# Optimization experiments

Hardware: AMD Instinct MI355X
Metric: run time of the kernel (lower is better)

Reference implementation:

```python
import jax, jax.numpy as jnp
import numpy as np

HEADS = 8
DIM_HEAD = 64
DIM = 128
TOPK = (8, 8, 8)  # depth, height, width


def chan_ln(x, g, b):
    # channel layernorm over axis=1 (biased variance), eps added to std
    mean = jnp.mean(x, axis=1, keepdims=True)
    var = jnp.var(x, axis=1, keepdims=True)
    return g * (x - mean) / (jnp.sqrt(var) + 1e-6) + b


def l2norm(x):
    # F.normalize(dim=1): divide by max(||x||_2, eps)
    n = jnp.sqrt(jnp.sum(x * x, axis=1, keepdims=True))
    return x / jnp.maximum(n, 1e-12)


def _forward(query_source, context, w_q, w_kv, w_out,
             ctx_gamma, ctx_beta, qs_gamma, qs_beta, out_gamma, out_beta, gamma):
    b, c, Dq, Hq, Wq = query_source.shape
    Dc, Hc, Wc = context.shape[2:]
    kd, kh, kw = TOPK

    ctx = chan_ln(context, ctx_gamma, ctx_beta)
    qs = chan_ln(query_source, qs_gamma, qs_beta)

    # 1x1x1 convs == channel matmuls
    kv = jnp.einsum('bcdhw,oc->bodhw', ctx, w_kv)   # (b, 2*inner, D, H, W)
    k, v = jnp.split(kv, 2, axis=1)
    q = jnp.einsum('bcdhw,oc->bodhw', qs, w_q)      # (b, inner, D, H, W)

    def fold(t):  # (b, h*c, D,H,W) -> (b*h, c, D,H,W)
        return t.reshape(b * HEADS, DIM_HEAD, *t.shape[2:])

    q, k, v = fold(q), fold(k), fold(v)
    q, k = l2norm(q), l2norm(k)

    q_probe = jnp.sum(q, axis=(2, 3, 4))            # (bh, c)
    k_abs = jnp.abs(k)

    if kd < Dc:
        score = jnp.einsum('bc,bcd->bd', q_probe, jnp.sum(k_abs, axis=(3, 4)))
        idx = jax.lax.top_k(score, kd)[1][:, None, :, None, None]
        k = jnp.take_along_axis(k, idx, axis=2)
        v = jnp.take_along_axis(v, idx, axis=2)
    if kh < Hc:
        score = jnp.einsum('bc,bch->bh', q_probe, jnp.sum(k_abs, axis=(2, 4)))
        idx = jax.lax.top_k(score, kh)[1][:, None, None, :, None]
        k = jnp.take_along_axis(k, idx, axis=3)
        v = jnp.take_along_axis(v, idx, axis=3)
    if kw < Wc:
        score = jnp.einsum('bc,bcw->bw', q_probe, jnp.sum(k_abs, axis=(2, 3)))
        idx = jax.lax.top_k(score, kw)[1][:, None, None, None, :]
        k = jnp.take_along_axis(k, idx, axis=4)
        v = jnp.take_along_axis(v, idx, axis=4)

    def flat(t):  # (bh, c, d, h, w) -> (bh, d*h*w, c)
        return t.reshape(t.shape[0], t.shape[1], -1).transpose(0, 2, 1)

    qf, kf, vf = flat(q), flat(k), flat(v)
    sim = jnp.einsum('bic,bjc->bij', qf, kf)        # (bh, Nq, Nkv)
    attn = jax.nn.softmax(sim, axis=-1)
    out = jnp.einsum('bij,bjc->bic', attn, vf)      # (bh, Nq, c)

    out = out.reshape(b, HEADS, Dq, Hq, Wq, DIM_HEAD)
    out = out.transpose(0, 1, 5, 2, 3, 4).reshape(b, HEADS * DIM_HEAD, Dq, Hq, Wq)
    out = jnp.einsum('bcdhw,oc->bodhw', out, w_out)
    out = chan_ln(out, out_gamma, out_beta)
    return gamma * out + query_source


def setup_inputs() -> dict:
    key = jax.random.key(0)
    ks = jax.random.split(key, 6)
    b, c, D, H, W = 2, DIM, 16, 32, 32
    inner = HEADS * DIM_HEAD
    ones = jnp.ones((1, c, 1, 1, 1), jnp.float32)
    zeros = jnp.zeros((1, c, 1, 1, 1), jnp.float32)
    return {
        'query_source': jax.random.normal(ks[0], (b, c, D, H, W), jnp.float32),
        'context': jax.random.normal(ks[1], (b, c, D, H, W), jnp.float32),
        'w_q': jax.random.normal(ks[2], (inner, c), jnp.float32) / np.sqrt(c).astype(np.float32),
        'w_kv': jax.random.normal(ks[3], (2 * inner, c), jnp.float32) / np.sqrt(c).astype(np.float32),
        'w_out': jax.random.normal(ks[4], (c, inner), jnp.float32) / np.sqrt(inner).astype(np.float32),
        'ctx_gamma': ones, 'ctx_beta': zeros,
        'qs_gamma': ones, 'qs_beta': zeros,
        'out_gamma': ones, 'out_beta': zeros,
        'gamma': jnp.full((1,), 0.5, jnp.float32),
    }


def reference(query_source, context, w_q, w_kv, w_out,
              ctx_gamma, ctx_beta, qs_gamma, qs_beta, out_gamma, out_beta, gamma):
    return _forward(query_source, context, w_q, w_kv, w_out,
                    ctx_gamma, ctx_beta, qs_gamma, qs_beta, out_gamma, out_beta, gamma)
```

## Files before the change

### kernel.cpp

```cpp
#include <hip/hip_runtime.h>
#include <hip/hip_bf16.h>

#define S_SP 16384
#define NKV 512

typedef short short8 __attribute__((ext_vector_type(8)));
typedef float v4f   __attribute__((ext_vector_type(4)));

__device__ __forceinline__ unsigned short f2bf(float x){
  union { float f; unsigned u; } v; v.f = x;
  unsigned r = v.u + 0x7FFFu + ((v.u >> 16) & 1u);
  return (unsigned short)(r >> 16);
}
__device__ __forceinline__ float bf2f(unsigned short h){
  union { unsigned u; float f; } v; v.u = ((unsigned)h) << 16; return v.f;
}

#if defined(__has_builtin)
#if __has_builtin(__builtin_amdgcn_cvt_pk_bf16_f32)
#define HAVE_PKBF 1
#endif
#endif

__device__ __forceinline__ unsigned pk2(float a, float b){
#ifdef HAVE_PKBF
  typedef __bf16 bf16x2 __attribute__((ext_vector_type(2)));
  union { bf16x2 v; unsigned u; } r;
  r.v = __builtin_amdgcn_cvt_pk_bf16_f32(a, b);
  return r.u;
#else
  return (unsigned)f2bf(a) | ((unsigned)f2bf(b) << 16);
#endif
}

__device__ __forceinline__ short8 u2s8(uint4 u){
  union { uint4 u; short8 s; } x; x.u = u; return x.s;
}

__global__ __launch_bounds__(256) void k_stats(const float* __restrict__ ctx,
                                               const float* __restrict__ qs,
                                               const float* __restrict__ ctx_g,
                                               const float* __restrict__ ctx_b,
                                               const float* __restrict__ qs_g,
                                               const float* __restrict__ qs_b,
                                               const float* __restrict__ wq,
                                               const float* __restrict__ wkv,
                                               float* __restrict__ MEAN,
                                               float* __restrict__ INV,
                                               unsigned short* __restrict__ XTC_hi,
                                               unsigned short* __restrict__ XTC_lo,
                                               unsigned short* __restrict__ XTQ_hi,
                                               unsigned short* __restrict__ XTQ_lo,
                                               unsigned short* __restrict__ WQh,
                                               unsigned short* __restrict__ WQl,
                                               unsigned short* __restrict__ WKh,
                                               unsigned short* __restrict__ WKl){
  __shared__ float r1[4][64];
  __shared__ float r2[4][64];
  __shared__ float mb[64], ib[64];
  __shared__ __align__(16) unsigned short TH[64*136];
  __shared__ __align__(16) unsigned short TL[64*136];
  int bx = blockIdx.x;
  int t = threadIdx.x;
  if (bx >= 1024){
    int wb = bx - 1024;
    int isK = wb >> 5;
    size_t i8 = ((size_t)(wb & 31)*256 + t)*8;
    const float* srcw = isK ? wkv : wq;
    unsigned short* dh = isK ? WKh : WQh;
    unsigned short* dl = isK ? WKl : WQl;
    v4f a  = *(const v4f*)(srcw + i8);
    v4f b2 = *(const v4f*)(srcw + i8 + 4);
    unsigned short h[8], l[8];
    #pragma unroll
    for (int i=0;i<4;i++){
      h[i]   = f2bf(a[i]);  l[i]   = f2bf(a[i]  - bf2f(h[i]));
      h[i+4] = f2bf(b2[i]); l[i+4] = f2bf(b2[i] - bf2f(h[i+4]));
    }
    uint4 uh, ul;
    uh.x = (unsigned)h[0] | ((unsigned)h[1]<<16);
    uh.y = (unsigned)h[2] | ((unsigned)h[3]<<16);
    uh.z = (unsigned)h[4] | ((unsigned)h[5]<<16);
    uh.w = (unsigned)h[6] | ((unsigned)h[7]<<16);
    ul.x = (unsigned)l[0] | ((unsigned)l[1]<<16);
    ul.y = (unsigned)l[2] | ((unsigned)l[3]<<16);
    ul.z = (unsigned)l[4] | ((unsigned)l[5]<<16);
    ul.w = (unsigned)l[6] | ((unsigned)l[7]<<16);
    *(uint4*)(dh + i8) = uh;
    *(uint4*)(dl + i8) = ul;
    return;
  }
  int tt = bx >> 9; int b = (bx >> 8) & 1; int sc = bx & 255;
  int sv = t & 63, cg = t >> 6;
  int s = sc*64 + sv;
  const float* src = (tt ? qs : ctx) + ((size_t)b*128 + cg*32)*S_SP + s;
  const float* G  = tt ? qs_g : ctx_g;
  const float* Bv = tt ? qs_b : ctx_b;
  float xv[32];
  float sum = 0.f, ss = 0.f;
  #pragma unroll
  for (int c = 0; c < 32; c++){
    float v = src[(size_t)c*S_SP];
    xv[c] = v;
    sum += v; ss += v*v;
  }
  r1[cg][sv] = sum; r2[cg][sv] = ss;
  __syncthreads();
  if (t < 64){
    float sm = r1[0][t]+r1[1][t]+r1[2][t]+r1[3][t];
    float sq = r2[0][t]+r2[1][t]+r2[2][t]+r2[3][t];
    float mean = sm * 0.0078125f;
    float var  = fmaxf(sq * 0.0078125f - mean*mean, 0.f);
    float inv  = 1.f/(sqrtf(var) + 1e-6f);
    int o = tt*2*S_SP + b*S_SP + sc*64 + t;
    MEAN[o] = mean; INV[o] = inv;
    mb[t] = mean; ib[t] = inv;
  }
  __syncthreads();
  float m = mb[sv], iv = ib[sv];
  #pragma unroll
  for (int i = 0; i < 32; i += 2){
    int c = cg*32 + i;
    float y0 = G[c]  *(xv[i]  -m)*iv + Bv[c];
    float y1 = G[c+1]*(xv[i+1]-m)*iv + Bv[c+1];
    unsigned short h0 = f2bf(y0), h1 = f2bf(y1);
    unsigned short l0 = f2bf(y0 - bf2f(h0)), l1 = f2bf(y1 - bf2f(h1));
    *(unsigned*)&TH[sv*136 + c] = (unsigned)h0 | ((unsigned)h1 << 16);
    *(unsigned*)&TL[sv*136 + c] = (unsigned)l0 | ((unsigned)l1 << 16);
  }
  __syncthreads();
  int row = t >> 2, seg = (t & 3) * 32;
  unsigned short* XH = tt ? XTQ_hi : XTC_hi;
  unsigned short* XL = tt ? XTQ_lo : XTC_lo;
  size_t go = ((size_t)b*S_SP + sc*64 + row)*128 + seg;
  #pragma unroll
  for (int k2 = 0; k2 < 4; k2++){
    *(uint4*)(XH + go + k2*8) = *(const uint4*)&TH[row*136 + seg + k2*8];
    *(uint4*)(XL + go + k2*8) = *(const uint4*)&TL[row*136 + seg + k2*8];
  }
}

template<int ISK>
__global__ __launch_bounds__(256, 2) void k_proj(
    const unsigned short* __restrict__ XH, const unsigned short* __restrict__ XL,
    const unsigned short* __restrict__ WH, const unsigned short* __restrict__ WL,
    unsigned short* __restrict__ QBF, float* __restrict__ QP,
    float* __restrict__ SCORE){
  __shared__ float qpl[128];
  __shared__ float qacc[128];
  __shared__ float wacc[64];
  int bx = blockIdx.x;
  int og = bx >> 7, b = (bx >> 6) & 1, stile = bx & 63;
  int t = threadIdx.x, wvi = t >> 6, lane = t & 63;
  int quad = lane >> 4, l15 = lane & 15;
  int sw0 = stile*256 + wvi*64;
  int bh0 = b*8 + og*2;
  if (ISK){
    if (t < 128) qpl[t] = QP[bh0*64 + t];
    if (t < 64) wacc[t] = 0.f;
    __syncthreads();
  } else {
    if (t < 128) qacc[t] = 0.f;
  }
  v4f acc[8][4];
  #pragma unroll
  for (int i=0;i<8;i++)
    #pragma unroll
    for (int j=0;j<4;j++) acc[i][j] = (v4f){0.f,0.f,0.f,0.f};
  size_t wrow = ((size_t)(og*128 + l15))*128 + quad*8;
  size_t xrow = ((size_t)b*S_SP + sw0 + l15)*128 + quad*8;
  #pragma unroll 1
  for (int ks=0; ks<4; ks++){
    int ko = ks*32;
    uint4 bhv[4], blv[4], av[8];
    #pragma unroll
    for (int nt=0;nt<4;nt++){
      bhv[nt] = *(const uint4*)(XH + xrow + nt*2048 + ko);
      blv[nt] = *(const uint4*)(XL + xrow + nt*2048 + ko);
    }
    #pragma unroll
    for (int mt=0;mt<8;mt++) av[mt] = *(const uint4*)(WH + wrow + mt*2048 + ko);
    #pragma unroll
    for (int mt=0;mt<8;mt++){
      short8 am = u2s8(av[mt]);
      #pragma unroll
      for (int nt=0;nt<4;nt++)
        acc[mt][nt] = __builtin_amdgcn_mfma_f32_16x16x32_bf16(am, u2s8(bhv[nt]), acc[mt][nt], 0, 0, 0);
      #pragma unroll
      for (int nt=0;nt<4;nt++)
        acc[mt][nt] = __builtin_amdgcn_mfma_f32_16x16x32_bf16(am, u2s8(blv[nt]), acc[mt][nt], 0, 0, 0);
    }
    #pragma unroll
    for (int mt=0;mt<8;mt++){
      short8 am = u2s8(*(const uint4*)(WL + wrow + mt*2048 + ko));
      #pragma unroll
      for (int nt=0;nt<4;nt++)
        acc[mt][nt] = __builtin_amdgcn_mfma_f32_16x16x32_bf16(am, u2s8(bhv[nt]), acc[mt][nt], 0, 0, 0);
    }
  }
  float inv0[4], inv1[4];
  #pragma unroll
  for (int nt=0;nt<4;nt++){
    float p0 = 0.f, p1 = 0.f;
    #pragma unroll
    for (int mt=0;mt<4;mt++)
      #pragma unroll
      for (int r=0;r<4;r++){
        p0 += acc[mt][nt][r]*acc[mt][nt][r];
        p1 += acc[mt+4][nt][r]*acc[mt+4][nt][r];
      }
    p0 += __shfl_xor(p0,16,64); p0 += __shfl_xor(p0,32,64);
    p1 += __shfl_xor(p1,16,64); p1 += __shfl_xor(p1,32,64);
    inv0[nt] = 1.f/fmaxf(sqrtf(p0),1e-12f);
    inv1[nt] = 1.f/fmaxf(sqrtf(p1),1e-12f);
  }
  if (!ISK){
    #pragma unroll
    for (int mt=0;mt<8;mt++)
      #pragma unroll
      for (int nt=0;nt<4;nt++){
        float iv = (mt<4) ? inv0[nt] : inv1[nt];
        #pragma unroll
        for (int r=0;r<4;r++) acc[mt][nt][r] *= iv;
      }
    #pragma unroll
    for (int mt=0;mt<8;mt++){
      int bh = bh0 + (mt>>2);
      #pragma unroll
      for (int nt=0;nt<4;nt++){
        int s = sw0 + nt*16 + l15;
        uint2 wv;
        wv.x = pk2(acc[mt][nt][0], acc[mt][nt][1]);
        wv.y = pk2(acc[mt][nt][2], acc[mt][nt][3]);
        *(uint2*)(QBF + ((size_t)bh*S_SP + s)*64 + (mt&3)*16 + quad*4) = wv;
      }
    }
    __syncthreads();
    #pragma unroll
    for (int mt=0;mt<8;mt++){
      #pragma unroll
      for (int r=0;r<4;r++){
        float v = acc[mt][0][r]+acc[mt][1][r]+acc[mt][2][r]+acc[mt][3][r];
        v += __shfl_xor(v,1,64); v += __shfl_xor(v,2,64);
        v += __shfl_xor(v,4,64); v += __shfl_xor(v,8,64);
        if (l15 == 0)
          atomicAdd(&qacc[(mt>>2)*64 + (mt&3)*16 + quad*4 + r], v);
      }
    }
    __syncthreads();
    if (t < 128) atomicAdd(QP + bh0*64 + t, qacc[t]);
  } else {
    float v0[4] = {0,0,0,0}, v1[4] = {0,0,0,0};
    #pragma unroll
    for (int mt=0;mt<8;mt++){
      #pragma unroll
      for (int r=0;r<4;r++){
        float w = qpl[mt*16 + quad*4 + r];
        #pragma unroll
        for (int nt=0;nt<4;nt++){
          float av = fabsf(acc[mt][nt][r]) * w;
          if (mt < 4) v0[nt] += av; else v1[nt] += av;
        }
      }
    }
    #pragma unroll
    for (int nt=0;nt<4;nt++){
      v0[nt] += __shfl_xor(v0[nt],16,64); v0[nt] += __shfl_xor(v0[nt],32,64);
      v1[nt] += __shfl_xor(v1[nt],16,64); v1[nt] += __shfl_xor(v1[nt],32,64);
      v0[nt] *= inv0[nt]; v1[nt] *= inv1[nt];
    }
    float w00 = v0[0]+v0[2], w10 = v0[1]+v0[3];
    float w01 = v1[0]+v1[2], w11 = v1[1]+v1[3];
    float h00 = v0[0]+v0[1], h01 = v0[2]+v0[3];
    float h10 = v1[0]+v1[1], h11 = v1[2]+v1[3];
    #pragma unroll
    for (int mm=1; mm<16; mm<<=1){
      h00 += __shfl_xor(h00,mm,64); h01 += __shfl_xor(h01,mm,64);
      h10 += __shfl_xor(h10,mm,64); h11 += __shfl_xor(h11,mm,64);
    }
    if (lane < 16){
      atomicAdd(&wacc[l15],      w00);
      atomicAdd(&wacc[16+l15],   w10);
      atomicAdd(&wacc[32+l15],   w01);
      atomicAdd(&wacc[48+l15],   w11);
    }
    if (lane == 0){
      int hb = 16 + (stile&3)*8 + wvi*2;
      atomicAdd(SCORE + bh0*80 + hb,     h00);
      atomicAdd(SCORE + bh0*80 + hb + 1, h01);
      atomicAdd(SCORE + (bh0+1)*80 + hb,     h10);
      atomicAdd(SCORE + (bh0+1)*80 + hb + 1, h11);
      atomicAdd(SCORE + bh0*80 + (stile>>2), h00+h01);
      atomicAdd(SCORE + (bh0+1)*80 + (stile>>2), h10+h11);
    }
    __syncthreads();
    if (t < 64) atomicAdd(SCORE + (bh0 + (t>>5))*80 + 48 + (t&31), wacc[t]);
  }
}

__global__ __launch_bounds__(64) void k_topk(const float* __restrict__ SCORE,
                                             int* __restrict__ IDX){
  int bh = blockIdx.x;
  if (threadIdx.x != 0) return;
  float sc[80];
  for (int i=0;i<80;i++) sc[i] = SCORE[bh*80+i];
  for (int a=0;a<3;a++){
    int n = a ? 32 : 16;
    int off = (a==0) ? 0 : (a==1 ? 16 : 48);
    for (int it=0; it<8; it++){
      int bi = 0; float bv = -3.4e38f;
      for (int i=0;i<n;i++){ float v = sc[off+i]; if (v > bv){ bv=v; bi=i; } }
      IDX[bh*24 + a*8 + it] = bi;
      sc[off+bi] = -3.4e38f;
    }
  }
}

__global__ __launch_bounds__(256) void k_gather(const float* __restrict__ ctx,
    const float* __restrict__ wkv, const float* __restrict__ ctx_g,
    const float* __restrict__ ctx_b, const float* __restrict__ MEAN,
    const float* __restrict__ INV, const int* __restrict__ IDX,
    unsigned short* __restrict__ KG, unsigned short* __restrict__ VGT){
  __shared__ float wlds[64*129];
  __shared__ float xln[32*128];
  __shared__ int sidx[24];
  int bx = blockIdx.x;
  int bh = bx >> 5, jc = (bx >> 1) & 15, type = bx & 1;
  int head = bh & 7, b = bh >> 3;
  int t = threadIdx.x;
  if (t < 24) sidx[t] = IDX[bh*24 + t];
  {
    int oc = t>>2, ks = (t&3)*32;
    const float* wr = wkv + ((size_t)(type*512 + head*64 + oc))*128 + ks;
    #pragma unroll 8
    for (int i=0;i<32;i++) wlds[oc*129 + ks + i] = wr[i];
  }
  __syncthreads();
  {
    int jl = t>>3, seg = (t&7)*16;
    int jj = jc*32 + jl;
    int dsel = sidx[jj>>6], hsel = sidx[8 + ((jj>>3)&7)], wsel = sidx[16 + (jj&7)];
    int sj = dsel*1024 + hsel*32 + wsel;
    float mn = MEAN[b*S_SP + sj];
    float iv = INV[b*S_SP + sj];
    #pragma unroll
    for (int i=0;i<16;i++){
      int cc = seg + i;
      float raw = ctx[((size_t)(b*128 + cc))*S_SP + sj];
      xln[jl*128 + cc] = ctx_g[cc]*(raw - mn)*iv + ctx_b[cc];
    }
  }
  __syncthreads();
  int c = t & 63, jg = t >> 6;
  float accv[8] = {};
  #pragma unroll 4
  for (int k=0;k<128;k++){
    float wv = wlds[c*129 + k];
    #pragma unroll
    for (int m=0;m<8;m++) accv[m] += wv * xln[(jg + 4*m)*128 + k];
  }
  #pragma unroll
  for (int m=0;m<8;m++){
    int jj = jc*32 + jg + 4*m;
    float a = accv[m];
    if (type == 0){
      float sq = a*a;
      #pragma unroll
      for (int mm=32; mm; mm>>=1) sq += __shfl_xor(sq, mm, 64);
      float rn = 1.f/fmaxf(sqrtf(sq), 1e-12f);
      KG[((size_t)bh*NKV + jj)*64 + c] = f2bf(a*rn);
    } else {
      VGT[((size_t)bh*64 + c)*NKV + jj] = f2bf(a);
    }
  }
}

__global__ __launch_bounds__(256) void k_attn(const unsigned short* __restrict__ QBF,
    const unsigned short* __restrict__ KG, const unsigned short* __restrict__ VGT,
    unsigned short* __restrict__ AOUT){
  __shared__ __align__(16) unsigned short kst[128*72];
  __shared__ __align__(16) unsigned short vst[64*136];
  __shared__ __align__(16) unsigned short pst[4][64*40];
  int bx = blockIdx.x;
  int bh = bx >> 6, qb = bx & 63;
  int t = threadIdx.x;
  int wvi = t >> 6, lane = t & 63;
  int quad = lane >> 4, l15 = lane & 15;
  int q0 = qb*256 + wvi*64;
  const unsigned short* kgb = KG + (size_t)bh*NKV*64;
  const unsigned short* vgb = VGT + (size_t)bh*64*NKV;
  short8 bq[4][2];
  #pragma unroll
  for (int qt=0; qt<4; qt++){
    const unsigned short* qp_ = QBF + ((size_t)bh*S_SP + q0 + qt*16 + l15)*64 + quad*8;
    union { uint4 u; short8 s; } u0, u1;
    u0.u = *(const uint4*)(qp_);
    u1.u = *(const uint4*)(qp_ + 32);
    bq[qt][0] = u0.s; bq[qt][1] = u1.s;
  }
  v4f oacc[4][4];
  #pragma unroll
  for (int i=0;i<4;i++)
    #pragma unroll
    for (int j=0;j<4;j++) oacc[i][j] = (v4f){0.f,0.f,0.f,0.f};
  float lsum[4] = {0.f,0.f,0.f,0.f};
  unsigned short* pw = pst[wvi];
  for (int ch=0; ch<4; ch++){
    __syncthreads();
    {
      int jl = t>>1, hf = (t&1)*32;
      const unsigned short* sp = kgb + (size_t)(ch*128 + jl)*64 + hf;
      unsigned short* dp = kst + jl*72 + hf;
      #pragma unroll
      for (int i=0;i<4;i++) *(uint4*)(dp + i*8) = *(const uint4*)(sp + i*8);
    }
    {
      int cc = t>>2, js = (t&3)*32;
      const unsigned short* sp = vgb + (size_t)cc*NKV + ch*128 + js;
      unsigned short* dp = vst + cc*136 + js;
      #pragma unroll
      for (int i=0;i<4;i++) *(uint4*)(dp + i*8) = *(const uint4*)(sp + i*8);
    }
    __syncthreads();
    #pragma unroll
    for (int sub=0; sub<4; sub++){
      v4f s[2][4];
      #pragma unroll
      for (int j2=0; j2<2; j2++){
        int jt = sub*2 + j2;
        const unsigned short* kr = kst + (jt*16 + l15)*72 + quad*8;
        union { uint4 u; short8 s; } a0, a1;
        a0.u = *(const uint4*)(kr);
        a1.u = *(const uint4*)(kr + 32);
        #pragma unroll
        for (int qt=0; qt<4; qt++){
          v4f z = {0.f,0.f,0.f,0.f};
          z = __builtin_amdgcn_mfma_f32_16x16x32_bf16(a0.s, bq[qt][0], z, 0, 0, 0);
          z = __builtin_amdgcn_mfma_f32_16x16x32_bf16(a1.s, bq[qt][1], z, 0, 0, 0);
          s[j2][qt] = z;
        }
      }
      #pragma unroll
      for (int j2=0; j2<2; j2++){
        #pragma unroll
        for (int qt=0; qt<4; qt++){
          v4f p;
          #pragma unroll
          for (int r=0;r<4;r++) p[r] = __expf(s[j2][qt][r] - 1.0f);
          lsum[qt] += p[0]+p[1]+p[2]+p[3];
          uint2 wv;
          wv.x = pk2(p[0], p[1]);
          wv.y = pk2(p[2], p[3]);
          *(uint2*)&pw[(qt*16 + l15)*40 + j2*16 + quad*4] = wv;
        }
      }
      short8 bp[4];
      #pragma unroll
      for (int qt=0; qt<4; qt++){
        union { uint4 u; short8 s; } ub;
        ub.u = *(const uint4*)&pw[(qt*16 + l15)*40 + quad*8];
        bp[qt] = ub.s;
      }
      #pragma unroll
      for (int ct=0; ct<4; ct++){
        union { uint4 u; short8 s; } av;
        av.u = *(const uint4*)&vst[(ct*16 + l15)*136 + sub*32 + quad*8];
        #pragma unroll
        for (int qt=0; qt<4; qt++)
          oacc[ct][qt] = __builtin_amdgcn_mfma_f32_16x16x32_bf16(av.s, bp[qt], oacc[ct][qt], 0, 0, 0);
      }
    }
  }
  float rl[4];
  #pragma unroll
  for (int qt=0; qt<4; qt++){
    float l = lsum[qt];
    l += __shfl_xor(l, 16, 64);
    l += __shfl_xor(l, 32, 64);
    rl[qt] = 1.f/l;
  }
  #pragma unroll
  for (int qt=0; qt<4; qt++){
    #pragma unroll
    for (int ct=0; ct<4; ct++){
      v4f o = oacc[ct][qt];
      uint2 wv;
      wv.x = pk2(o[0]*rl[qt], o[1]*rl[qt]);
      wv.y = pk2(o[2]*rl[qt], o[3]*rl[qt]);
      *(uint2*)(AOUT + ((size_t)bh*S_SP + q0 + qt*16 + l15)*64 + ct*16 + quad*4) = wv;
    }
  }
}

__global__ __launch_bounds__(256) void k_out(const unsigned short* __restrict__ AOUT,
    const float* __restrict__ wout, const float* __restrict__ out_g,
    const float* __restrict__ out_b, const float* __restrict__ gamma,
    const float* __restrict__ qsrc, float* __restrict__ OUT){
  __shared__ __align__(16) unsigned short wl[128*40];
  __shared__ float lnp[4][2][64];
  __shared__ float mbuf[64], sbuf[64], ogl[128], obl[128];
  int bx = blockIdx.x; int b = bx>>8; int stile = bx&255; int s0 = stile*64;
  int t = threadIdx.x; int w = t>>6; int lane = t&63;
  int q = lane>>4; int l15 = lane&15;
  if (t < 128){ ogl[t] = out_g[t]; obl[t] = out_b[t]; }
  v4f acc[2][4];
  #pragma unroll
  for (int i=0;i<2;i++)
    #pragma unroll
    for (int j=0;j<4;j++) acc[i][j] = (v4f){0.f,0.f,0.f,0.f};
  for (int kt=0; kt<16; kt++){
    __syncthreads();
    {
      int c = t>>1, kb = (t&1)*16;
      const float* wr = wout + (size_t)c*512 + kt*32 + kb;
      v4f a0 = *(const v4f*)wr, a1 = *(const v4f*)(wr+4);
      v4f a2 = *(const v4f*)(wr+8), a3 = *(const v4f*)(wr+12);
      uint4 u0, u1;
      u0.x = pk2(a0[0], a0[1]); u0.y = pk2(a0[2], a0[3]);
      u0.z = pk2(a1[0], a1[1]); u0.w = pk2(a1[2], a1[3]);
      u1.x = pk2(a2[0], a2[1]); u1.y = pk2(a2[2], a2[3]);
      u1.z = pk2(a3[0], a3[1]); u1.w = pk2(a3[2], a3[3]);
      *(uint4*)&wl[c*40+kb]   = u0;
      *(uint4*)&wl[c*40+kb+8] = u1;
    }
    __syncthreads();
    short8 af[2];
    #pragma unroll
    for (int mt=0;mt<2;mt++){
      union { uint4 u; short8 s; } ua;
      ua.u = *(const uint4*)&wl[(w*32+mt*16+l15)*40 + q*8];
      af[mt] = ua.s;
    }
    int head = kt>>1; int cc0 = (kt&1)*32 + q*8;
    const unsigned short* bp = AOUT + ((size_t)((b*8+head)*S_SP + s0 + l15))*64 + cc0;
    #pragma unroll
    for (int nt=0;nt<4;nt++){
      union { uint4 u; short8 s; } ub;
      ub.u = *(const uint4*)(bp + (size_t)nt*16*64);
      #pragma unroll
      for (int mt=0;mt<2;mt++)
        acc[mt][nt] = __builtin_amdgcn_mfma_f32_16x16x32_bf16(af[mt], ub.s, acc[mt][nt], 0, 0, 0);
    }
  }
  #pragma unroll
  for (int nt=0;nt<4;nt++){
    float p1 = 0.f, p2 = 0.f;
    #pragma unroll
    for (int mt=0;mt<2;mt++)
      #pragma unroll
      for (int r=0;r<4;r++){ float v = acc[mt][nt][r]; p1 += v; p2 += v*v; }
    p1 += __shfl_xor(p1,16,64); p1 += __shfl_xor(p1,32,64);
    p2 += __shfl_xor(p2,16,64); p2 += __shfl_xor(p2,32,64);
    if (q == 0){ lnp[w][0][nt*16+l15] = p1; lnp[w][1][nt*16+l15] = p2; }
  }
  __syncthreads();
  if (t < 64){
    float m = (lnp[0][0][t]+lnp[1][0][t]+lnp[2][0][t]+lnp[3][0][t]) * 0.0078125f;
    float qq = (lnp[0][1][t]+lnp[1][1][t]+lnp[2][1][t]+lnp[3][1][t]) * 0.0078125f;
    float var = fmaxf(qq - m*m, 0.f);
    mbuf[t] = m;
    sbuf[t] = 1.f/(sqrtf(var) + 1e-6f);
  }
  __syncthreads();
  float gs = gamma[0];
  #pragma unroll
  for (int nt=0;nt<4;nt++){
    int sl = nt*16 + l15;
    float mm = mbuf[sl], ssc = sbuf[sl];
    #pragma unroll
    for (int mt=0;mt<2;mt++){
      #pragma unroll
      for (int r=0;r<4;r++){
        int c = w*32 + mt*16 + q*4 + r;
        size_t adr = ((size_t)(b*128+c))*S_SP + s0 + sl;
        float yn = (acc[mt][nt][r]-mm)*ssc;
        OUT[adr] = gs*(ogl[c]*yn + obl[c]) + qsrc[adr];
      }
    }
  }
}

extern "C" void kernel_launch(void* const* d_in, const int* in_sizes, int n_in,
                              void* d_out, int out_size, void* d_ws, size_t ws_size,
                              hipStream_t stream){
  const float* qsrc  = (const float*)d_in[0];
  const float* ctx   = (const float*)d_in[1];
  const float* wq    = (const float*)d_in[2];
  const float* wkv   = (const float*)d_in[3];
  const float* wout  = (const float*)d_in[4];
  const float* ctx_g = (const float*)d_in[5];
  const float* ctx_b = (const float*)d_in[6];
  const float* qs_g  = (const float*)d_in[7];
  const float* qs_b  = (const float*)d_in[8];
  const float* out_g = (const float*)d_in[9];
  const float* out_b = (const float*)d_in[10];
  const float* gamma = (const float*)d_in[11];
  float* OUT = (float*)d_out;
  char* ws = (char*)d_ws;
  float* QP    = (float*)(ws);
  float* SCORE = (float*)(ws + 4096);
  float* MEAN  = (float*)(ws + 16384);
  float* INV   = (float*)(ws + 278528);
  int*   IDX   = (int*)(ws + 540672);
  unsigned short* QBF  = (unsigned short*)(ws + 544768);
  unsigned short* KG   = (unsigned short*)(ws + 34099200);
  unsigned short* VGT  = (unsigned short*)(ws + 35147776);
  unsigned short* AOUT = (unsigned short*)(ws + 36196352);
  unsigned short* WQh = (unsigned short*)(ws + 34099200);
  unsigned short* WQl = (unsigned short*)(ws + 34230272);
  unsigned short* WKh = (unsigned short*)(ws + 34361344);
  unsigned short* WKl = (unsigned short*)(ws + 34492416);
  unsigned short* XTQh = (unsigned short*)(ws + 36196352);
  unsigned short* XTQl = (unsigned short*)(ws + 44584960);
  unsigned short* XTCh = (unsigned short*)(ws + 52973568);
  unsigned short* XTCl = (unsigned short*)(ws + 61362176);

  hipMemsetAsync(ws, 0, 9216, stream);
  k_stats<<<1088, 256, 0, stream>>>(ctx, qsrc, ctx_g, ctx_b, qs_g, qs_b, wq, wkv,
                                    MEAN, INV, XTCh, XTCl, XTQh, XTQl,
                                    WQh, WQl, WKh, WKl);
  k_proj<0><<<512, 256, 0, stream>>>(XTQh, XTQl, WQh, WQl, QBF, QP, SCORE);
  k_proj<1><<<512, 256, 0, stream>>>(XTCh, XTCl, WKh, WKl, QBF, QP, SCORE);
  k_topk<<<16, 64, 0, stream>>>(SCORE, IDX);
  k_gather<<<512, 256, 0, stream>>>(ctx, wkv, ctx_g, ctx_b, MEAN, INV, IDX, KG, VGT);
  k_attn<<<1024, 256, 0, stream>>>(QBF, KG, VGT, AOUT);
  k_out<<<512, 256, 0, stream>>>(AOUT, wout, out_g, out_b, gamma, qsrc, OUT);
}
```

Baseline: 304.5 us.

## Fuse top-k into gather kernel, swizzle attention LDS, raise MFMA priority

The separate single-thread top-k kernel is removed. Each gather block now recomputes the top-k indices with a wave-level shuffle argmax, which saves a launch and a serial loop at the cost of redundant work in every block. The attention kernel drops its padded LDS layouts for XOR-swizzled unpadded layouts for K, V and P, aiming to avoid bank conflicts with less shared memory. It also wraps MFMA sequences in s_setprio to favour the matrix work.

```diff
diff --git a/kernel.cpp b/kernel.cpp
--- a/kernel.cpp
+++ b/kernel.cpp
@@ -298,42 +298,46 @@
   }
 }
 
-__global__ __launch_bounds__(64) void k_topk(const float* __restrict__ SCORE,
-                                             int* __restrict__ IDX){
-  int bh = blockIdx.x;
-  if (threadIdx.x != 0) return;
-  float sc[80];
-  for (int i=0;i<80;i++) sc[i] = SCORE[bh*80+i];
-  for (int a=0;a<3;a++){
-    int n = a ? 32 : 16;
-    int off = (a==0) ? 0 : (a==1 ? 16 : 48);
-    for (int it=0; it<8; it++){
-      int bi = 0; float bv = -3.4e38f;
-      for (int i=0;i<n;i++){ float v = sc[off+i]; if (v > bv){ bv=v; bi=i; } }
-      IDX[bh*24 + a*8 + it] = bi;
-      sc[off+bi] = -3.4e38f;
-    }
-  }
-}
-
 __global__ __launch_bounds__(256) void k_gather(const float* __restrict__ ctx,
     const float* __restrict__ wkv, const float* __restrict__ ctx_g,
     const float* __restrict__ ctx_b, const float* __restrict__ MEAN,
-    const float* __restrict__ INV, const int* __restrict__ IDX,
+    const float* __restrict__ INV, const float* __restrict__ SCORE,
     unsigned short* __restrict__ KG, unsigned short* __restrict__ VGT){
   __shared__ float wlds[64*129];
   __shared__ float xln[32*128];
+  __shared__ float scb[80];
   __shared__ int sidx[24];
   int bx = blockIdx.x;
   int bh = bx >> 5, jc = (bx >> 1) & 15, type = bx & 1;
   int head = bh & 7, b = bh >> 3;
   int t = threadIdx.x;
-  if (t < 24) sidx[t] = IDX[bh*24 + t];
+  if (t < 80) scb[t] = SCORE[bh*80 + t];
   {
     int oc = t>>2, ks = (t&3)*32;
     const float* wr = wkv + ((size_t)(type*512 + head*64 + oc))*128 + ks;
     #pragma unroll 8
     for (int i=0;i<32;i++) wlds[oc*129 + ks + i] = wr[i];
+  }
+  __syncthreads();
+  if (t < 64){
+    #pragma unroll 1
+    for (int a=0;a<3;a++){
+      int n = a ? 32 : 16;
+      int off = (a==0) ? 0 : (a==1 ? 16 : 48);
+      float v = (t < n) ? scb[off+t] : -3.4e38f;
+      #pragma unroll 1
+      for (int it=0; it<8; it++){
+        float bv = v; int bi = t;
+        #pragma unroll
+        for (int mm=1; mm<32; mm<<=1){
+          float ov = __shfl_xor(bv, mm, 64);
+          int oi = __shfl_xor(bi, mm, 64);
+          if (ov > bv || (ov == bv && oi < bi)){ bv = ov; bi = oi; }
+        }
+        if (t == bi) v = -3.4e38f;
+        if (t == 0) sidx[a*8+it] = bi;
+      }
+    }
   }
   __syncthreads();
   {
@@ -378,9 +382,9 @@
 __global__ __launch_bounds__(256) void k_attn(const unsigned short* __restrict__ QBF,
     const unsigned short* __restrict__ KG, const unsigned short* __restrict__ VGT,
     unsigned short* __restrict__ AOUT){
-  __shared__ __align__(16) unsigned short kst[128*72];
-  __shared__ __align__(16) unsigned short vst[64*136];
-  __shared__ __align__(16) unsigned short pst[4][64*40];
+  __shared__ __align__(16) unsigned short kst[128*64];
+  __shared__ __align__(16) unsigned short vst[64*128];
+  __shared__ __align__(16) unsigned short pst[4][64*32];
   int bx = blockIdx.x;
   int bh = bx >> 6, qb = bx & 63;
   int t = threadIdx.x;
@@ -408,18 +412,20 @@
   for (int ch=0; ch<4; ch++){
     __syncthreads();
     {
-      int jl = t>>1, hf = (t&1)*32;
-      const unsigned short* sp = kgb + (size_t)(ch*128 + jl)*64 + hf;
-      unsigned short* dp = kst + jl*72 + hf;
-      #pragma unroll
-      for (int i=0;i<4;i++) *(uint4*)(dp + i*8) = *(const uint4*)(sp + i*8);
+      int jl = t>>1, bb = (t&1)*4;
+      const unsigned short* sp = kgb + (size_t)(ch*128 + jl)*64 + (t&1)*32;
+      unsigned short* dp = kst + jl*64;
+      int sw = jl & 7;
+      #pragma unroll
+      for (int i=0;i<4;i++) *(uint4*)(dp + (((bb+i)^sw)*8)) = *(const uint4*)(sp + i*8);
     }
     {
-      int cc = t>>2, js = (t&3)*32;
-      const unsigned short* sp = vgb + (size_t)cc*NKV + ch*128 + js;
-      unsigned short* dp = vst + cc*136 + js;
-      #pragma unroll
-      for (int i=0;i<4;i++) *(uint4*)(dp + i*8) = *(const uint4*)(sp + i*8);
+      int cc = t>>2, bb = (t&3)*4;
+      const unsigned short* sp = vgb + (size_t)cc*NKV + ch*128 + (t&3)*32;
+      unsigned short* dp = vst + cc*128;
+      int sw = cc & 7;
+      #pragma unroll
+      for (int i=0;i<4;i++) *(uint4*)(dp + (((bb+i)^sw)*8)) = *(const uint4*)(sp + i*8);
     }
     __syncthreads();
     #pragma unroll
@@ -427,11 +433,13 @@
       v4f s[2][4];
       #pragma unroll
       for (int j2=0; j2<2; j2++){
-        int jt = sub*2 + j2;
-        const unsigned short* kr = kst + (jt*16 + l15)*72 + quad*8;
+        int jr = (sub*2 + j2)*16 + l15;
+        const unsigned short* kr = kst + jr*64;
+        int sk = jr & 7;
         union { uint4 u; short8 s; } a0, a1;
-        a0.u = *(const uint4*)(kr);
-        a1.u = *(const uint4*)(kr + 32);
+        a0.u = *(const uint4*)(kr + ((quad^sk)*8));
+        a1.u = *(const uint4*)(kr + (((quad+4)^sk)*8));
+        __builtin_amdgcn_s_setprio(1);
         #pragma unroll
         for (int qt=0; qt<4; qt++){
           v4f z = {0.f,0.f,0.f,0.f};
@@ -439,6 +447,7 @@
           z = __builtin_amdgcn_mfma_f32_16x16x32_bf16(a1.s, bq[qt][1], z, 0, 0, 0);
           s[j2][qt] = z;
         }
+        __builtin_amdgcn_s_setprio(0);
       }
       #pragma unroll
       for (int j2=0; j2<2; j2++){
@@ -451,23 +460,28 @@
           uint2 wv;
           wv.x = pk2(p[0], p[1]);
           wv.y = pk2(p[2], p[3]);
-          *(uint2*)&pw[(qt*16 + l15)*40 + j2*16 + quad*4] = wv;
+          int qr = qt*16 + l15;
+          *(uint2*)&pw[qr*32 + (((j2*2+(quad>>1))^(qr&3))*8) + (quad&1)*4] = wv;
         }
       }
       short8 bp[4];
       #pragma unroll
       for (int qt=0; qt<4; qt++){
+        int qr = qt*16 + l15;
         union { uint4 u; short8 s; } ub;
-        ub.u = *(const uint4*)&pw[(qt*16 + l15)*40 + quad*8];
+        ub.u = *(const uint4*)&pw[qr*32 + ((quad^(qr&3))*8)];
         bp[qt] = ub.s;
       }
       #pragma unroll
       for (int ct=0; ct<4; ct++){
+        int cr = ct*16 + l15;
         union { uint4 u; short8 s; } av;
-        av.u = *(const uint4*)&vst[(ct*16 + l15)*136 + sub*32 + quad*8];
+        av.u = *(const uint4*)&vst[cr*128 + (((sub*4+quad)^(cr&7))*8)];
+        __builtin_amdgcn_s_setprio(1);
         #pragma unroll
         for (int qt=0; qt<4; qt++)
           oacc[ct][qt] = __builtin_amdgcn_mfma_f32_16x16x32_bf16(av.s, bp[qt], oacc[ct][qt], 0, 0, 0);
+        __builtin_amdgcn_s_setprio(0);
       }
     }
   }
@@ -601,7 +615,6 @@
   float* SCORE = (float*)(ws + 4096);
   float* MEAN  = (float*)(ws + 16384);
   float* INV   = (float*)(ws + 278528);
-  int*   IDX   = (int*)(ws + 540672);
   unsigned short* QBF  = (unsigned short*)(ws + 544768);
   unsigned short* KG   = (unsigned short*)(ws + 34099200);
   unsigned short* VGT  = (unsigned short*)(ws + 35147776);
@@ -621,8 +634,7 @@
                                     WQh, WQl, WKh, WKl);
   k_proj<0><<<512, 256, 0, stream>>>(XTQh, XTQl, WQh, WQl, QBF, QP, SCORE);
   k_proj<1><<<512, 256, 0, stream>>>(XTCh, XTCl, WKh, WKl, QBF, QP, SCORE);
-  k_topk<<<16, 64, 0, stream>>>(SCORE, IDX);
-  k_gather<<<512, 256, 0, stream>>>(ctx, wkv, ctx_g, ctx_b, MEAN, INV, IDX, KG, VGT);
+  k_gather<<<512, 256, 0, stream>>>(ctx, wkv, ctx_g, ctx_b, MEAN, INV, SCORE, KG, VGT);
   k_attn<<<1024, 256, 0, stream>>>(QBF, KG, VGT, AOUT);
   k_out<<<512, 256, 0, stream>>>(AOUT, wout, out_g, out_b, gamma, qsrc, OUT);
 }
```

Result: no change. 300.2 us (median of 2 runs) (-1.4%).
